# Optimization experiments

Measured on AMD Instinct MI355X. Metric: run time of the kernel, lower is better.

The kernel has to match this reference:

```python
import jax, jax.numpy as jnp
import numpy as np

Z, K, H, Y = 128, 256, 512, 4  # z_size, key_size, hidden_size, y_dim


def setup_inputs() -> dict:
    key = jax.random.key(0)
    ks = jax.random.split(key, 8)
    B, T, P = 512, 32, 32
    s = lambda k, shape, sc: (jax.random.normal(k, shape, jnp.float32) * sc)
    return {
        "x_seq": jax.random.normal(ks[0], (B, T, P, P), jnp.float32),
        "W_enc": s(ks[1], (P * P, Z), 0.03),
        "gamma": jnp.ones((Z,), jnp.float32),
        "beta": jnp.zeros((Z,), jnp.float32),
        "W_ih": s(ks[2], (4 * H, K + 1), 0.05),
        "W_hh": s(ks[3], (4 * H, H), 0.04),
        "b_ih": jnp.zeros((4 * H,), jnp.float32),
        "b_hh": jnp.zeros((4 * H,), jnp.float32),
        "W_key": s(ks[4], (K, H), 0.06),
        "b_key": jnp.zeros((K,), jnp.float32),
        "W_g": s(ks[5], (1, H), 0.06),
        "b_g": jnp.zeros((1,), jnp.float32),
        "conf_gain": jnp.ones((1,), jnp.float32),
        "conf_bias": jnp.zeros((1,), jnp.float32),
        "W_y": s(ks[6], (Y, H), 0.06),
        "b_y": jnp.zeros((Y,), jnp.float32),
    }


def _lstm_cell(x, h, c, W_ih, W_hh, b_ih, b_hh):
    # PyTorch gate order: i, f, g, o
    gates = x @ W_ih.T + b_ih + h @ W_hh.T + b_hh
    i, f, g, o = jnp.split(gates, 4, axis=-1)
    c = jax.nn.sigmoid(f) * c + jax.nn.sigmoid(i) * jnp.tanh(g)
    h = jax.nn.sigmoid(o) * jnp.tanh(c)
    return h, c


def _forward(x_seq, W_enc, gamma, beta, W_ih, W_hh, b_ih, b_hh,
             W_key, b_key, W_g, b_g, conf_gain, conf_bias, W_y, b_y):
    B, T, P, _ = x_seq.shape
    # encoder: flatten -> linear to z_size (stand-in for Encoder_mlp)
    z = x_seq.reshape(B, T, P * P) @ W_enc  # [B, T, Z]
    # context norm over the sequence dim (single task segment)
    mu = z.mean(axis=1, keepdims=True)
    sig = jnp.sqrt(z.var(axis=1, keepdims=True) + 1e-8)
    z = (z - mu) / sig * gamma + beta

    M = T + 1  # T+1 steps; final step feeds a zero z_t
    z_pad = jnp.concatenate([z, jnp.zeros((B, 1, Z), z.dtype)], axis=1)  # [B, M, Z]

    h0 = jnp.zeros((B, H), z.dtype)
    c0 = jnp.zeros((B, H), z.dtype)
    kr0 = jnp.zeros((B, K + 1), z.dtype)
    Mk0 = jnp.zeros((B, M, K), z.dtype)
    Mv0 = jnp.zeros((B, M, Z), z.dtype)

    def step(carry, t):
        h, c, key_r, M_k, M_v = carry
        z_t = jax.lax.dynamic_index_in_dim(z_pad, t, axis=1, keepdims=False)  # [B, Z]
        h, c = _lstm_cell(key_r, h, c, W_ih, W_hh, b_ih, b_hh)
        key_w = jax.nn.relu(h @ W_key.T + b_key)          # [B, K]
        g = jax.nn.sigmoid(h @ W_g.T + b_g)               # [B, 1]
        y_lin = h @ W_y.T + b_y                            # [B, Y]
        # attention read over valid memory slots j < t
        scores = jnp.einsum('bz,bmz->bm', z_t, M_v)        # [B, M]
        valid = (jnp.arange(M) < t)[None, :]
        w_k = jax.nn.softmax(jnp.where(valid, scores, -1e9), axis=1)
        c_k = jax.nn.sigmoid(scores * conf_gain + conf_bias)
        kv = jnp.concatenate([M_k, c_k[..., None]], axis=2)  # [B, M, K+1]
        attn = g * jnp.einsum('bm,bmd->bd', w_k, kv)          # [B, K+1]
        key_r_new = jnp.where(t == 0, jnp.zeros_like(attn), attn)
        # append to memory at slot t
        M_k = jax.lax.dynamic_update_slice_in_dim(M_k, key_w[:, None, :], t, axis=1)
        M_v = jax.lax.dynamic_update_slice_in_dim(M_v, z_t[:, None, :], t, axis=1)
        return (h, c, key_r_new, M_k, M_v), y_lin

    _, ys = jax.lax.scan(step, (h0, c0, kr0, Mk0, Mv0), jnp.arange(M))
    return ys[-1]  # y_pred_linear from final step, [B, Y]


def reference(x_seq, W_enc, gamma, beta, W_ih, W_hh, b_ih, b_hh,
              W_key, b_key, W_g, b_g, conf_gain, conf_bias, W_y, b_y):
    y_pred_linear = _forward(x_seq, W_enc, gamma, beta, W_ih, W_hh, b_ih, b_hh,
                             W_key, b_key, W_g, b_g, conf_gain, conf_bias, W_y, b_y)
    y_pred = jnp.argmax(y_pred_linear, axis=1)
    return y_pred_linear, y_pred
```

## Files before the change

### kernel.cpp

```cpp
#include <hip/hip_runtime.h>
#include <math.h>

typedef unsigned short ushort;
typedef unsigned int uint;
typedef __bf16 bf16x8 __attribute__((ext_vector_type(8)));
typedef float f32x4 __attribute__((ext_vector_type(4)));

#define ZS    128
#define KS    256
#define HS    512
#define BATCH 512
#define TT    32
#define MM    33
#define NB    2304
#define KPAD  800
#define HOFF  272
#define LDA   800

static __device__ __forceinline__ float sigf(float x) { return 1.f / (1.f + expf(-x)); }
static __device__ __forceinline__ float bf2f(ushort u) { return __uint_as_float((uint)u << 16); }

__global__ void prep_w(const float* __restrict__ W_ih, const float* __restrict__ W_hh,
                       const float* __restrict__ W_key, const float* __restrict__ b_ih,
                       const float* __restrict__ b_hh, const float* __restrict__ b_key,
                       const float* __restrict__ W_enc,
                       ushort* __restrict__ Whi, ushort* __restrict__ Wlo,
                       ushort* __restrict__ Behi, ushort* __restrict__ Belo,
                       float* __restrict__ biasN)
{
    int idx = blockIdx.x * 256 + threadIdx.x;
    if (idx < NB) {
        float bv;
        if (idx < 2048) { int j = idx >> 2, gi = idx & 3, r = gi * 512 + j; bv = b_ih[r] + b_hh[r]; }
        else bv = b_key[idx - 2048];
        biasN[idx] = bv;
    }
    if (idx < NB * KPAD) {
        int n = idx / KPAD, k = idx - n * KPAD;
        float v = 0.f;
        if (n < 2048) {
            int j = n >> 2, gi = n & 3, r = gi * 512 + j;
            if (k < 257) v = W_ih[r * 257 + k];
            else if (k >= HOFF && k < HOFF + 512) v = W_hh[r * 512 + (k - HOFF)];
        } else {
            if (k >= HOFF && k < HOFF + 512) v = W_key[(n - 2048) * 512 + (k - HOFF)];
        }
        uint u = __float_as_uint(v);
        Whi[idx] = (ushort)(u >> 16);
        float lo = v - __uint_as_float(u & 0xFFFF0000u);
        Wlo[idx] = (ushort)(__float_as_uint(lo) >> 16);
    } else if (idx < NB * KPAD + 128 * 1024) {
        int e = idx - NB * KPAD;
        int n = e >> 10, k = e & 1023;
        float v = W_enc[k * 128 + n];
        uint u = __float_as_uint(v);
        Behi[e] = (ushort)(u >> 16);
        float lo = v - __uint_as_float(u & 0xFFFF0000u);
        Belo[e] = (ushort)(__float_as_uint(lo) >> 16);
    }
}

#define LOADG_M(s, avf_, avu_, bhv_, blv_) do {                                   \
    const int k0 = (s) * 32;                                                      \
    if (PRESPLIT) {                                                               \
        int idx = tid & 127, r = idx >> 2, c = (idx & 3) << 3;                    \
        const ushort* srcp = (tid < 128) ? Ahi : Alo;                             \
        avu_ = *(const uint4*)(srcp + (size_t)(row0 + r) * lda + k0 + c);         \
    } else {                                                                      \
        int r = tid >> 3, c = (tid & 7) << 2;                                     \
        avf_ = *(const float4*)(A + (size_t)(row0 + r) * lda + k0 + c);           \
    }                                                                             \
    _Pragma("unroll")                                                             \
    for (int i = 0; i < BN / 64; i++) {                                           \
        int idx2 = tid + 256 * i, r2 = idx2 >> 2, c2 = (idx2 & 3) << 3;           \
        bhv_[i] = *(const uint4*)(Bhi + (size_t)(n0 + r2) * ldb + k0 + c2);       \
        blv_[i] = *(const uint4*)(Blo + (size_t)(n0 + r2) * ldb + k0 + c2);       \
    }                                                                             \
} while (0)

#define STORE_M(buf, avf_, avu_, bhv_, blv_) do {                                 \
    ushort* Lw = lds + (buf) * BUF;                                               \
    if (PRESPLIT) {                                                               \
        int idx = tid & 127, r = idx >> 2, c = (idx & 3) << 3;                    \
        *(uint4*)&Lw[(tid < 128 ? AHI : ALO) + r * 40 + c] = avu_;                \
    } else {                                                                     \
        int r = tid >> 3, c = (tid & 7) << 2;                                    \
        uint u0 = __float_as_uint(avf_.x), u1 = __float_as_uint(avf_.y);          \
        uint u2 = __float_as_uint(avf_.z), u3 = __float_as_uint(avf_.w);          \
        uint hp0 = (u1 & 0xFFFF0000u) | (u0 >> 16);                               \
        uint hp1 = (u3 & 0xFFFF0000u) | (u2 >> 16);                               \
        float l0 = avf_.x - __uint_as_float(u0 & 0xFFFF0000u);                    \
        float l1 = avf_.y - __uint_as_float(u1 & 0xFFFF0000u);                    \
        float l2 = avf_.z - __uint_as_float(u2 & 0xFFFF0000u);                    \
        float l3 = avf_.w - __uint_as_float(u3 & 0xFFFF0000u);                    \
        uint lp0 = (__float_as_uint(l1) & 0xFFFF0000u) | (__float_as_uint(l0) >> 16); \
        uint lp1 = (__float_as_uint(l3) & 0xFFFF0000u) | (__float_as_uint(l2) >> 16); \
        *(uint2*)&Lw[AHI + r * 40 + c] = make_uint2(hp0, hp1);                    \
        *(uint2*)&Lw[ALO + r * 40 + c] = make_uint2(lp0, lp1);                    \
    }                                                                             \
    _Pragma("unroll")                                                             \
    for (int i = 0; i < BN / 64; i++) {                                           \
        int idx3 = tid + 256 * i, r3 = idx3 >> 2, c3 = (idx3 & 3) << 3;           \
        *(uint4*)&Lw[BHI + r3 * 40 + c3] = bhv_[i];                               \
        *(uint4*)&Lw[BLO + r3 * 40 + c3] = blv_[i];                               \
    }                                                                             \
} while (0)

template<int BN, int MODE, bool PRESPLIT>
__global__ __launch_bounds__(256, (MODE == 0) ? 3 : 4)
void gemm_mfma(const float* __restrict__ A,
               const ushort* __restrict__ Ahi, const ushort* __restrict__ Alo, int lda,
               const ushort* __restrict__ Bhi, const ushort* __restrict__ Blo, int ldb,
               int nslice,
               float* __restrict__ out,
               ushort* __restrict__ outHi, ushort* __restrict__ outLo,
               const float* __restrict__ biasN,
               float* __restrict__ cst, float* __restrict__ Mk, int step)
{
    constexpr int NI = BN / 32;
    constexpr int AHI = 0, ALO = 32 * 40, BHI = 64 * 40, BLO = 64 * 40 + BN * 40;
    constexpr int BUF = 64 * 40 + 2 * BN * 40;
    __shared__ ushort lds[2 * BUF];

    const int tid = threadIdx.x;
    int bx, by;
    if (MODE == 1) {
        int wg = blockIdx.x;
        int swz = (wg & 7) * 72 + (wg >> 3);
        bx = swz >> 4; by = swz & 15;
    } else {
        bx = blockIdx.x; by = blockIdx.y;
        A   += (size_t)blockIdx.z * 512;
        Bhi += (size_t)blockIdx.z * 512;
        Blo += (size_t)blockIdx.z * 512;
        if (blockIdx.z) out = Mk;
    }
    const int row0 = by * 32, n0 = bx * BN;
    const int l = tid & 63, w = tid >> 6, wm = w >> 1, wn = w & 1;
    const int lm = l & 15, kg = (l >> 4) << 3;

    f32x4 acc[NI];
    const f32x4 zero4 = {0.f, 0.f, 0.f, 0.f};
#pragma unroll
    for (int ni = 0; ni < NI; ni++) acc[ni] = zero4;

    float4 avf0, avf1;
    uint4 avu0, avu1;
    uint4 bhv0[BN / 64], blv0[BN / 64], bhv1[BN / 64], blv1[BN / 64];

    auto COMPUTE = [&](int s) {
        const ushort* L = lds + (s & 1) * BUF;
        bf16x8 ah, alv, bh[NI], bl[NI];
        {
            int r = wm * 16 + lm;
            ah  = *(const bf16x8*)&L[AHI + r * 40 + kg];
            alv = *(const bf16x8*)&L[ALO + r * 40 + kg];
        }
#pragma unroll
        for (int ni = 0; ni < NI; ni++) {
            int r = wn * (BN / 2) + ni * 16 + lm;
            bh[ni] = *(const bf16x8*)&L[BHI + r * 40 + kg];
            bl[ni] = *(const bf16x8*)&L[BLO + r * 40 + kg];
        }
#pragma unroll
        for (int ni = 0; ni < NI; ni++) {
            acc[ni] = __builtin_amdgcn_mfma_f32_16x16x32_bf16(ah,  bh[ni], acc[ni], 0, 0, 0);
            acc[ni] = __builtin_amdgcn_mfma_f32_16x16x32_bf16(ah,  bl[ni], acc[ni], 0, 0, 0);
            acc[ni] = __builtin_amdgcn_mfma_f32_16x16x32_bf16(alv, bh[ni], acc[ni], 0, 0, 0);
        }
    };

    LOADG_M(0, avf0, avu0, bhv0, blv0);
    STORE_M(0, avf0, avu0, bhv0, blv0);
    if (nslice > 1) LOADG_M(1, avf1, avu1, bhv1, blv1);
    for (int s = 0; s < nslice; s += 2) {
        if (s + 2 < nslice) LOADG_M(s + 2, avf0, avu0, bhv0, blv0);
        __syncthreads();
        COMPUTE(s);
        if (s + 1 < nslice) STORE_M((s + 1) & 1, avf1, avu1, bhv1, blv1);
        if (s + 3 < nslice) LOADG_M(s + 3, avf1, avu1, bhv1, blv1);
        __syncthreads();
        if (s + 1 < nslice) {
            COMPUTE(s + 1);
            if (s + 2 < nslice) STORE_M((s + 2) & 1, avf0, avu0, bhv0, blv0);
        }
    }

    const int crow = (l >> 4) << 2;
    if (MODE == 0) {
#pragma unroll
        for (int ni = 0; ni < NI; ni++)
#pragma unroll
            for (int r = 0; r < 4; r++) {
                int m = row0 + wm * 16 + crow + r;
                int z = n0 + wn * (BN / 2) + ni * 16 + lm;
                out[(size_t)(m >> 5) * (MM * ZS) + (m & 31) * ZS + z] = acc[ni][r];
            }
    } else if (bx < 32) {
        __syncthreads();
        float* epi = (float*)lds;
        float* ew = epi + w * 544;
#pragma unroll
        for (int ni = 0; ni < NI; ni++)
#pragma unroll
            for (int r = 0; r < 4; r++) {
                int ml = crow + r, nl = ni * 16 + lm;
                ew[ml * 34 + nl] = acc[ni][r] + biasN[n0 + wn * 32 + nl];
            }
        __syncthreads();
        int row = tid >> 3, jj8 = tid & 7;
        int b = row0 + row;
        int j0 = bx * 16 + jj8 * 2;
        float2 cold = *(float2*)&cst[(size_t)b * HS + j0];
        float cc[2] = {cold.x, cold.y}, hv[2];
#pragma unroll
        for (int i = 0; i < 2; i++) {
            int jj = jj8 * 2 + i;
            float p[4];
#pragma unroll
            for (int g = 0; g < 4; g++) {
                int n = jj * 4 + g;
                int wv = (row >> 4) * 2 + (n >> 5);
                p[g] = epi[wv * 544 + (row & 15) * 34 + (n & 31)];
            }
            float ig = sigf(p[0]), fg = sigf(p[1]), gg = tanhf(p[2]), og = sigf(p[3]);
            float cn = fg * cc[i] + ig * gg;
            hv[i] = og * tanhf(cn);
            cc[i] = cn;
        }
        *(float2*)&cst[(size_t)b * HS + j0] = make_float2(cc[0], cc[1]);
        uint u0 = __float_as_uint(hv[0]), u1 = __float_as_uint(hv[1]);
        uint hp = (u1 & 0xFFFF0000u) | (u0 >> 16);
        float l0 = hv[0] - __uint_as_float(u0 & 0xFFFF0000u);
        float l1 = hv[1] - __uint_as_float(u1 & 0xFFFF0000u);
        uint lp = (__float_as_uint(l1) & 0xFFFF0000u) | (__float_as_uint(l0) >> 16);
        *(uint*)&outHi[(size_t)b * LDA + HOFF + j0] = hp;
        *(uint*)&outLo[(size_t)b * LDA + HOFF + j0] = lp;
    } else if (step >= 1) {
#pragma unroll
        for (int ni = 0; ni < NI; ni++)
#pragma unroll
            for (int r = 0; r < 4; r++) {
                int b = row0 + wm * 16 + crow + r;
                int cg = n0 + wn * 32 + ni * 16 + lm;
                float v = fmaxf(acc[ni][r] + biasN[cg], 0.f);
                Mk[((size_t)(step - 1) * BATCH + b) * KS + (cg - 2048)] = v;
            }
    }
}

#undef LOADG_M
#undef STORE_M

__global__ void norm_k(float* __restrict__ z_pad, const float* __restrict__ z2,
                       const float* __restrict__ gamma, const float* __restrict__ beta)
{
    int b = blockIdx.x, zc = threadIdx.x;
    float* zb = z_pad + (size_t)b * (MM * ZS);
    const float* zb2 = z2 + (size_t)b * (MM * ZS);
    float s = 0.f, s2 = 0.f;
    for (int t = 0; t < TT; t++) {
        float v = zb[t * ZS + zc] + zb2[t * ZS + zc];
        zb[t * ZS + zc] = v;
        s += v; s2 += v * v;
    }
    float mu = s * (1.f / 32.f);
    float var = s2 * (1.f / 32.f) - mu * mu;
    float rstd = 1.f / sqrtf(var + 1e-8f);
    float ga = gamma[zc], be = beta[zc];
    for (int t = 0; t < TT; t++) {
        float v = zb[t * ZS + zc];
        zb[t * ZS + zc] = (v - mu) * rstd * ga + be;
    }
    zb[TT * ZS + zc] = 0.f;
}

__global__ __launch_bounds__(256)
void scores_k(const float* __restrict__ z_pad, const float* __restrict__ cg_p,
              const float* __restrict__ cb_p, float* __restrict__ watt,
              float* __restrict__ wc)
{
    __shared__ float zs[MM * 129];
    int b = blockIdx.x, tid = threadIdx.x;
    const float* zb = z_pad + (size_t)b * (MM * ZS);
    for (int i = tid; i < MM * ZS; i += 256) {
        int m = i >> 7, k = i & 127;
        zs[m * 129 + k] = zb[i];
    }
    __syncthreads();
    float cg = cg_p[0], cb = cb_p[0];
    int wid = tid >> 6, lane = tid & 63;
    for (int t = 1 + wid; t <= 32; t += 4) {
        int m = lane;
        float s = -3.0e38f;
        if (m < t) {
            const float* zt = &zs[t * 129];
            const float* zm = &zs[m * 129];
            float acc = 0.f;
#pragma unroll 8
            for (int k = 0; k < ZS; k++) acc += zt[k] * zm[k];
            s = acc;
        }
        float mx = s;
        for (int off = 1; off < 64; off <<= 1) mx = fmaxf(mx, __shfl_xor(mx, off));
        float e = (m < t) ? expf(s - mx) : 0.f;
        float sum = e;
        for (int off = 1; off < 64; off <<= 1) sum += __shfl_xor(sum, off);
        float w = e / sum;
        if (m < t) watt[(b * MM + t) * MM + m] = w;
        float p = (m < t) ? w * sigf(s * cg + cb) : 0.f;
        for (int off = 1; off < 64; off <<= 1) p += __shfl_xor(p, off);
        if (lane == 0) wc[b * MM + t] = p;
    }
}

__global__ __launch_bounds__(256)
void post_k(ushort* __restrict__ inpHi, ushort* __restrict__ inpLo,
            const float* __restrict__ W_g, const float* __restrict__ b_g,
            const float* __restrict__ watt, const float* __restrict__ wc,
            const float* __restrict__ Mk, int t)
{
    __shared__ float red[256];
    __shared__ float wts[32];
    __shared__ float gsh;
    int b = blockIdx.x, tid = threadIdx.x;
    ushort* rHi = inpHi + (size_t)b * LDA;
    ushort* rLo = inpLo + (size_t)b * LDA;
    float h1 = bf2f(rHi[HOFF + tid]) + bf2f(rLo[HOFF + tid]);
    float h2 = bf2f(rHi[HOFF + 256 + tid]) + bf2f(rLo[HOFF + 256 + tid]);
    red[tid] = h1 * W_g[tid] + h2 * W_g[tid + 256];
    if (tid < t) wts[tid] = watt[(b * MM + t) * MM + tid];
    __syncthreads();
    for (int s = 128; s > 0; s >>= 1) {
        if (tid < s) red[tid] += red[tid + s];
        __syncthreads();
    }
    if (tid == 0) gsh = sigf(red[0] + b_g[0]);
    __syncthreads();
    float g = gsh;
    float acc = 0.f;
    for (int m = 0; m < t; m++)
        acc += wts[m] * Mk[((size_t)m * BATCH + b) * KS + tid];
    float v = g * acc;
    uint u = __float_as_uint(v);
    rHi[tid] = (ushort)(u >> 16);
    float lo = v - __uint_as_float(u & 0xFFFF0000u);
    rLo[tid] = (ushort)(__float_as_uint(lo) >> 16);
    if (tid == 0) {
        float vc = g * wc[b * MM + t];
        uint uc = __float_as_uint(vc);
        rHi[256] = (ushort)(uc >> 16);
        float lc = vc - __uint_as_float(uc & 0xFFFF0000u);
        rLo[256] = (ushort)(__float_as_uint(lc) >> 16);
    }
}

__global__ void y_k(const ushort* __restrict__ inpHi, const ushort* __restrict__ inpLo,
                    const float* __restrict__ W_y, const float* __restrict__ b_y,
                    float* __restrict__ out)
{
    int b = blockIdx.x, lane = threadIdx.x;
    const ushort* hHi = inpHi + (size_t)b * LDA + HOFF;
    const ushort* hLo = inpLo + (size_t)b * LDA + HOFF;
    float a0 = 0, a1 = 0, a2 = 0, a3 = 0;
    for (int r = 0; r < 8; r++) {
        int k = lane + r * 64;
        float hv = bf2f(hHi[k]) + bf2f(hLo[k]);
        a0 += hv * W_y[k];
        a1 += hv * W_y[512 + k];
        a2 += hv * W_y[1024 + k];
        a3 += hv * W_y[1536 + k];
    }
    for (int off = 32; off > 0; off >>= 1) {
        a0 += __shfl_xor(a0, off);
        a1 += __shfl_xor(a1, off);
        a2 += __shfl_xor(a2, off);
        a3 += __shfl_xor(a3, off);
    }
    if (lane == 0) {
        float y0 = a0 + b_y[0], y1 = a1 + b_y[1], y2 = a2 + b_y[2], y3 = a3 + b_y[3];
        out[b * 4 + 0] = y0; out[b * 4 + 1] = y1; out[b * 4 + 2] = y2; out[b * 4 + 3] = y3;
        int best = 0; float bv = y0;
        if (y1 > bv) { bv = y1; best = 1; }
        if (y2 > bv) { bv = y2; best = 2; }
        if (y3 > bv) { bv = y3; best = 3; }
        out[2048 + b] = (float)best;
    }
}

extern "C" void kernel_launch(void* const* d_in, const int* in_sizes, int n_in,
                              void* d_out, int out_size, void* d_ws, size_t ws_size,
                              hipStream_t stream)
{
    const float* x_seq = (const float*)d_in[0];
    const float* W_enc = (const float*)d_in[1];
    const float* gamma = (const float*)d_in[2];
    const float* beta  = (const float*)d_in[3];
    const float* W_ih  = (const float*)d_in[4];
    const float* W_hh  = (const float*)d_in[5];
    const float* b_ih  = (const float*)d_in[6];
    const float* b_hh  = (const float*)d_in[7];
    const float* W_key = (const float*)d_in[8];
    const float* b_key = (const float*)d_in[9];
    const float* W_g   = (const float*)d_in[10];
    const float* b_g   = (const float*)d_in[11];
    const float* cgain = (const float*)d_in[12];
    const float* cbias = (const float*)d_in[13];
    const float* W_y   = (const float*)d_in[14];
    const float* b_y   = (const float*)d_in[15];

    float* ws    = (float*)d_ws;
    float* z_pad = ws;
    float* watt  = z_pad + 2162688;
    float* wcv   = watt + 557568;
    float* Mk    = wcv + 16896;
    float* biasN = Mk + 4194304;
    float* cst   = biasN + 2304;
    ushort* inpHi0 = (ushort*)(cst + 262144);
    ushort* inpLo0 = inpHi0 + 409600;
    ushort* inpHi1 = inpLo0 + 409600;
    ushort* inpLo1 = inpHi1 + 409600;
    ushort* Whi  = inpLo1 + 409600;
    ushort* Wlo  = Whi + NB * KPAD;
    ushort* Behi = Wlo + NB * KPAD;
    ushort* Belo = Behi + 131072;

    hipMemsetAsync(cst, 0, 262144 * sizeof(float) + 4 * 409600 * sizeof(ushort), stream);

    prep_w<<<(NB * KPAD + 131072 + 255) / 256, 256, 0, stream>>>(
        W_ih, W_hh, W_key, b_ih, b_hh, b_key, W_enc, Whi, Wlo, Behi, Belo, biasN);

    gemm_mfma<128, 0, false><<<dim3(1, 512, 2), 256, 0, stream>>>(
        x_seq, nullptr, nullptr, 1024, Behi, Belo, 1024, 16,
        z_pad, nullptr, nullptr, nullptr, nullptr, Mk, 0);
    norm_k<<<512, 128, 0, stream>>>(z_pad, Mk, gamma, beta);
    scores_k<<<512, 256, 0, stream>>>(z_pad, cgain, cbias, watt, wcv);

    for (int t = 0; t <= 32; t++) {
        ushort* inHiC = (t & 1) ? inpHi1 : inpHi0;
        ushort* inLoC = (t & 1) ? inpLo1 : inpLo0;
        ushort* inHiN = (t & 1) ? inpHi0 : inpHi1;
        ushort* inLoN = (t & 1) ? inpLo0 : inpLo1;
        gemm_mfma<64, 1, true><<<dim3(576), 256, 0, stream>>>(
            nullptr, inHiC, inLoC, LDA, Whi, Wlo, KPAD, 25,
            nullptr, inHiN, inLoN, biasN, cst, Mk, t);
        if (t >= 1 && t <= 31)
            post_k<<<512, 256, 0, stream>>>(inHiN, inLoN, W_g, b_g, watt, wcv, Mk, t);
    }
    y_k<<<512, 64, 0, stream>>>((0 ? inpHi0 : inpHi1), (0 ? inpLo0 : inpLo1),
                                W_y, b_y, (float*)d_out);
}
```

Before: 1.058 ms.

## Restructure GEMM K-loop into multi-slice windows with one barrier per window

Reworks the double-buffered K loop of the split-bf16 MFMA GEMM so each pipeline stage covers a window of NCH k-slices. The recurrent per-step GEMM now uses two slices per window, and the encoder GEMM uses one. The goal is to halve the number of __syncthreads per K pass and issue global loads for the next window before computing the current one. In exchange, LDS use doubles for the recurrent GEMM, more prefetch registers are live, and the encoder GEMM's launch bound rises from 3 to 4 blocks per SM, which may force register spills.

```diff
diff --git a/kernel.cpp b/kernel.cpp
--- a/kernel.cpp
+++ b/kernel.cpp
@@ -60,7 +60,7 @@
     }
 }
 
-#define LOADG_M(s, avf_, avu_, bhv_, blv_) do {                                   \
+#define LOADC_M(s, avf_, avu_, bhv_, blv_) do {                                   \
     const int k0 = (s) * 32;                                                      \
     if (PRESPLIT) {                                                               \
         int idx = tid & 127, r = idx >> 2, c = (idx & 3) << 3;                    \
@@ -78,13 +78,13 @@
     }                                                                             \
 } while (0)
 
-#define STORE_M(buf, avf_, avu_, bhv_, blv_) do {                                 \
-    ushort* Lw = lds + (buf) * BUF;                                               \
+#define STOREC_M(wb, ch, avf_, avu_, bhv_, blv_) do {                             \
+    ushort* Lw = lds + ((wb) * NCH + (ch)) * BUF_C;                               \
     if (PRESPLIT) {                                                               \
         int idx = tid & 127, r = idx >> 2, c = (idx & 3) << 3;                    \
         *(uint4*)&Lw[(tid < 128 ? AHI : ALO) + r * 40 + c] = avu_;                \
-    } else {                                                                     \
-        int r = tid >> 3, c = (tid & 7) << 2;                                    \
+    } else {                                                                      \
+        int r = tid >> 3, c = (tid & 7) << 2;                                     \
         uint u0 = __float_as_uint(avf_.x), u1 = __float_as_uint(avf_.y);          \
         uint u2 = __float_as_uint(avf_.z), u3 = __float_as_uint(avf_.w);          \
         uint hp0 = (u1 & 0xFFFF0000u) | (u0 >> 16);                               \
@@ -106,8 +106,8 @@
     }                                                                             \
 } while (0)
 
-template<int BN, int MODE, bool PRESPLIT>
-__global__ __launch_bounds__(256, (MODE == 0) ? 3 : 4)
+template<int BN, int MODE, bool PRESPLIT, int NCH>
+__global__ __launch_bounds__(256, 4)
 void gemm_mfma(const float* __restrict__ A,
                const ushort* __restrict__ Ahi, const ushort* __restrict__ Alo, int lda,
                const ushort* __restrict__ Bhi, const ushort* __restrict__ Blo, int ldb,
@@ -119,8 +119,8 @@
 {
     constexpr int NI = BN / 32;
     constexpr int AHI = 0, ALO = 32 * 40, BHI = 64 * 40, BLO = 64 * 40 + BN * 40;
-    constexpr int BUF = 64 * 40 + 2 * BN * 40;
-    __shared__ ushort lds[2 * BUF];
+    constexpr int BUF_C = 64 * 40 + 2 * BN * 40;
+    __shared__ ushort lds[2 * NCH * BUF_C];
 
     const int tid = threadIdx.x;
     int bx, by;
@@ -148,8 +148,8 @@
     uint4 avu0, avu1;
     uint4 bhv0[BN / 64], blv0[BN / 64], bhv1[BN / 64], blv1[BN / 64];
 
-    auto COMPUTE = [&](int s) {
-        const ushort* L = lds + (s & 1) * BUF;
+    auto COMPUTE = [&](int wb, int ch) {
+        const ushort* L = lds + (wb * NCH + ch) * BUF_C;
         bf16x8 ah, alv, bh[NI], bl[NI];
         {
             int r = wm * 16 + lm;
@@ -170,19 +170,22 @@
         }
     };
 
-    LOADG_M(0, avf0, avu0, bhv0, blv0);
-    STORE_M(0, avf0, avu0, bhv0, blv0);
-    if (nslice > 1) LOADG_M(1, avf1, avu1, bhv1, blv1);
-    for (int s = 0; s < nslice; s += 2) {
-        if (s + 2 < nslice) LOADG_M(s + 2, avf0, avu0, bhv0, blv0);
+    LOADC_M(0, avf0, avu0, bhv0, blv0);
+    if (NCH == 2 && 1 < nslice) LOADC_M(1, avf1, avu1, bhv1, blv1);
+    STOREC_M(0, 0, avf0, avu0, bhv0, blv0);
+    if (NCH == 2 && 1 < nslice) STOREC_M(0, 1, avf1, avu1, bhv1, blv1);
+
+    const int nwin = (nslice + NCH - 1) / NCH;
+    for (int wi = 0; wi < nwin; wi++) {
         __syncthreads();
-        COMPUTE(s);
-        if (s + 1 < nslice) STORE_M((s + 1) & 1, avf1, avu1, bhv1, blv1);
-        if (s + 3 < nslice) LOADG_M(s + 3, avf1, avu1, bhv1, blv1);
-        __syncthreads();
-        if (s + 1 < nslice) {
-            COMPUTE(s + 1);
-            if (s + 2 < nslice) STORE_M((s + 2) & 1, avf0, avu0, bhv0, blv0);
+        const int nb = (wi + 1) * NCH;
+        if (nb < nslice) LOADC_M(nb, avf0, avu0, bhv0, blv0);
+        if (NCH == 2 && nb + 1 < nslice) LOADC_M(nb + 1, avf1, avu1, bhv1, blv1);
+        COMPUTE(wi & 1, 0);
+        if (NCH == 2 && wi * NCH + 1 < nslice) COMPUTE(wi & 1, 1);
+        if (nb < nslice) {
+            STOREC_M((wi + 1) & 1, 0, avf0, avu0, bhv0, blv0);
+            if (NCH == 2 && nb + 1 < nslice) STOREC_M((wi + 1) & 1, 1, avf1, avu1, bhv1, blv1);
         }
     }
 
@@ -249,8 +252,8 @@
     }
 }
 
-#undef LOADG_M
-#undef STORE_M
+#undef LOADC_M
+#undef STOREC_M
 
 __global__ void norm_k(float* __restrict__ z_pad, const float* __restrict__ z2,
                        const float* __restrict__ gamma, const float* __restrict__ beta)
@@ -430,7 +433,7 @@
     prep_w<<<(NB * KPAD + 131072 + 255) / 256, 256, 0, stream>>>(
         W_ih, W_hh, W_key, b_ih, b_hh, b_key, W_enc, Whi, Wlo, Behi, Belo, biasN);
 
-    gemm_mfma<128, 0, false><<<dim3(1, 512, 2), 256, 0, stream>>>(
+    gemm_mfma<128, 0, false, 1><<<dim3(1, 512, 2), 256, 0, stream>>>(
         x_seq, nullptr, nullptr, 1024, Behi, Belo, 1024, 16,
         z_pad, nullptr, nullptr, nullptr, nullptr, Mk, 0);
     norm_k<<<512, 128, 0, stream>>>(z_pad, Mk, gamma, beta);
@@ -441,7 +444,7 @@
         ushort* inLoC = (t & 1) ? inpLo1 : inpLo0;
         ushort* inHiN = (t & 1) ? inpHi0 : inpHi1;
         ushort* inLoN = (t & 1) ? inpLo0 : inpLo1;
-        gemm_mfma<64, 1, true><<<dim3(576), 256, 0, stream>>>(
+        gemm_mfma<64, 1, true, 2><<<dim3(576), 256, 0, stream>>>(
             nullptr, inHiC, inLoC, LDA, Whi, Wlo, KPAD, 25,
             nullptr, inHiN, inLoN, biasN, cst, Mk, t);
         if (t >= 1 && t <= 31)
```

New measurement: 1.207 ms. 14.0% more time.
